# Optimization experiments

Hardware: AMD Instinct MI355X
Metric: run time of the kernel (lower is better)

The kernel has to match this reference:

```python
import jax, jax.numpy as jnp
import numpy as np

N = 100000      # nodes
E = 3200000     # edges
F_IN = 64       # num_input_features
HID = 3         # hardcoded hidden width in GCN
F_OUT = 256     # gcn_output_features
F_TR = 512      # transformer_feature_size


def setup_inputs() -> dict:
    key = jax.random.key(0)
    ks = jax.random.split(key, 12)
    x = jax.random.normal(ks[0], (N, F_IN), dtype=jnp.float32)
    edge_index = jax.random.randint(ks[1], (2, E), 0, N, dtype=jnp.int64)
    s = 0.05
    # ChebConv1 (K=2): two weight mats [in,out] + bias
    W0a = jax.random.normal(ks[2], (F_IN, HID), jnp.float32) * s
    W1a = jax.random.normal(ks[3], (F_IN, HID), jnp.float32) * s
    b1 = jax.random.normal(ks[4], (HID,), jnp.float32) * s
    # ChebConv2 (K=2)
    W0b = jax.random.normal(ks[5], (HID, F_OUT), jnp.float32) * s
    W1b = jax.random.normal(ks[6], (HID, F_OUT), jnp.float32) * s
    b2 = jax.random.normal(ks[7], (F_OUT,), jnp.float32) * s
    # final Linear
    Wl = jax.random.normal(ks[8], (F_OUT, F_TR), jnp.float32) * s
    bl = jax.random.normal(ks[9], (F_TR,), jnp.float32) * s
    return {"x": x, "edge_index": edge_index, "W0a": W0a, "W1a": W1a,
            "b1": b1, "W0b": W0b, "W1b": W1b, "b2": b2, "Wl": Wl, "bl": bl}


def _cheb_norm(edge_index, num_nodes):
    # PyG ChebConv.__norm__ with sym normalization, lambda_max=2.0:
    # L_hat = 2L/2 - I = -D^{-1/2} A D^{-1/2} (diagonal cancels to 0).
    src, dst = edge_index[0], edge_index[1]
    w = jnp.where(src != dst, 1.0, 0.0).astype(jnp.float32)  # remove_self_loops
    deg = jnp.zeros((num_nodes,), jnp.float32).at[src].add(w)
    dinv = jnp.where(deg > 0, jax.lax.rsqrt(jnp.maximum(deg, 1.0)), 0.0)
    return -dinv[src] * w * dinv[dst]  # [E]


def _cheb_conv(x, edge_index, norm, W0, W1, b):
    # K=2 Chebyshev: Tx0 = x, Tx1 = L_hat @ x (scatter-add over edges)
    src, dst = edge_index[0], edge_index[1]
    Tx1 = jnp.zeros_like(x).at[dst].add(norm[:, None] * x[src])
    return x @ W0 + Tx1 @ W1 + b


def reference(x, edge_index, W0a, W1a, b1, W0b, W1b, b2, Wl, bl):
    norm = _cheb_norm(edge_index, x.shape[0])
    h = jax.nn.relu(_cheb_conv(x, edge_index, norm, W0a, W1a, b1))
    h = jax.nn.relu(_cheb_conv(h, edge_index, norm, W0b, W1b, b2))
    return h @ Wl + bl
```

## Files before the change

kernel.cpp:

```cpp
#include <hip/hip_runtime.h>
#include <hip/hip_bf16.h>


#define MAXNB 1024
#define BSH 7
#define BSZ 128
#define SRC_BITS 20
#define SRC_MASK ((1u << SRC_BITS) - 1u)
#define EPB 16384

typedef __attribute__((ext_vector_type(8))) short short8;
typedef __attribute__((ext_vector_type(4))) float f32x4;

static __device__ inline unsigned short f2bf(float f) {
    union { float f; unsigned u; } v; v.f = f;
    unsigned r = (v.u + 0x7fffu + ((v.u >> 16) & 1u)) >> 16;
    return (unsigned short)r;
}

__global__ __launch_bounds__(256) void k_prep(const float* __restrict__ Wl,
                                              unsigned short* __restrict__ WlT,
                                              unsigned* __restrict__ subcurD,
                                              unsigned* __restrict__ subcurS) {
    __shared__ float tile[32][33];
    int t = threadIdx.x, tx = t & 31, ty = t >> 5;
    if (blockIdx.x == 0) {
        for (int i = t; i < MAXNB; i += 256) { subcurD[i] = 0u; subcurS[i] = 0u; }
    }
    int kb = (blockIdx.x & 7) * 32;
    int cb = (blockIdx.x >> 3) * 32;
#pragma unroll
    for (int r = 0; r < 4; r++) {
        int k = kb + ty + r * 8;
        tile[ty + r * 8][tx] = Wl[(size_t)k * 512 + cb + tx];
    }
    __syncthreads();
#pragma unroll
    for (int r = 0; r < 4; r++) {
        int c = cb + ty + r * 8;
        WlT[(size_t)c * 256 + kb + tx] = f2bf(tile[tx][ty + r * 8]);
    }
}

__global__ __launch_bounds__(1024) void k_hist(const int* __restrict__ ei, int E, int NB,
                                               unsigned* __restrict__ subcurD,
                                               unsigned* __restrict__ subcurS,
                                               unsigned* __restrict__ baseD,
                                               unsigned* __restrict__ baseS) {
    __shared__ unsigned hD[MAXNB], hS[MAXNB];
    int t = threadIdx.x, blk = blockIdx.x;
    for (int i = t; i < NB; i += 1024) { hD[i] = 0u; hS[i] = 0u; }
    __syncthreads();
    int e0 = blk * EPB, e1 = min(e0 + EPB, E);
    if ((E & 3) == 0) {
        int nv = (e1 - e0) >> 2;
        const int4* s4 = (const int4*)(ei + e0);
        const int4* d4 = (const int4*)(ei + (size_t)E + e0);
        for (int i = t; i < nv; i += 1024) {
            int4 ss = s4[i], dd = d4[i];
            if (ss.x != dd.x) { atomicAdd(&hD[dd.x >> BSH], 1u); atomicAdd(&hS[ss.x >> BSH], 1u); }
            if (ss.y != dd.y) { atomicAdd(&hD[dd.y >> BSH], 1u); atomicAdd(&hS[ss.y >> BSH], 1u); }
            if (ss.z != dd.z) { atomicAdd(&hD[dd.z >> BSH], 1u); atomicAdd(&hS[ss.z >> BSH], 1u); }
            if (ss.w != dd.w) { atomicAdd(&hD[dd.w >> BSH], 1u); atomicAdd(&hS[ss.w >> BSH], 1u); }
        }
        for (int e = e0 + (nv << 2) + t; e < e1; e += 1024) {
            int s = ei[e], d = ei[(size_t)E + e];
            if (s != d) { atomicAdd(&hD[d >> BSH], 1u); atomicAdd(&hS[s >> BSH], 1u); }
        }
    } else {
        for (int e = e0 + t; e < e1; e += 1024) {
            int s = ei[e], d = ei[(size_t)E + e];
            if (s != d) { atomicAdd(&hD[d >> BSH], 1u); atomicAdd(&hS[s >> BSH], 1u); }
        }
    }
    __syncthreads();
    unsigned* bD = baseD + (size_t)blk * NB;
    unsigned* bS = baseS + (size_t)blk * NB;
    for (int i = t; i < NB; i += 1024) {
        unsigned h = hD[i];
        if (h) bD[i] = atomicAdd(&subcurD[i], h);
        h = hS[i];
        if (h) bS[i] = atomicAdd(&subcurS[i], h);
    }
}

__global__ __launch_bounds__(1024) void k_scan(const unsigned* __restrict__ totD,
                                               const unsigned* __restrict__ totS,
                                               unsigned* __restrict__ startD,
                                               unsigned* __restrict__ startS, int NB) {
    __shared__ unsigned a[MAXNB], b[MAXNB];
    int t = threadIdx.x;
    for (int i = t; i < NB; i += 1024) a[i] = totD[i];
    __syncthreads();
    unsigned* s = a; unsigned* d = b;
    for (int off = 1; off < NB; off <<= 1) {
        for (int i = t; i < NB; i += 1024)
            d[i] = s[i] + (i >= off ? s[i - off] : 0u);
        __syncthreads();
        unsigned* tmp = s; s = d; d = tmp;
    }
    for (int i = t; i < NB; i += 1024)
        startD[i] = (i == 0) ? 0u : s[i - 1];
    if (t == 0) startD[NB] = s[NB - 1];
    __syncthreads();
    for (int i = t; i < NB; i += 1024) a[i] = totS[i];
    __syncthreads();
    s = a; d = b;
    for (int off = 1; off < NB; off <<= 1) {
        for (int i = t; i < NB; i += 1024)
            d[i] = s[i] + (i >= off ? s[i - off] : 0u);
        __syncthreads();
        unsigned* tmp = s; s = d; d = tmp;
    }
    for (int i = t; i < NB; i += 1024)
        startS[i] = (i == 0) ? 0u : s[i - 1];
    if (t == 0) startS[NB] = s[NB - 1];
}

__global__ __launch_bounds__(1024) void k_place(const int* __restrict__ ei, int E, int NB,
                                                const unsigned* __restrict__ startD,
                                                const unsigned* __restrict__ startS,
                                                const unsigned* __restrict__ baseD,
                                                const unsigned* __restrict__ baseS,
                                                unsigned* __restrict__ dstbin,
                                                unsigned char* __restrict__ srcbin) {
    __shared__ unsigned oD[MAXNB], oS[MAXNB], cD[MAXNB], cS[MAXNB];
    int t = threadIdx.x, blk = blockIdx.x;
    const unsigned* bD = baseD + (size_t)blk * NB;
    const unsigned* bS = baseS + (size_t)blk * NB;
    for (int i = t; i < NB; i += 1024) {
        oD[i] = startD[i] + bD[i];
        oS[i] = startS[i] + bS[i];
        cD[i] = 0u; cS[i] = 0u;
    }
    __syncthreads();
    int e0 = blk * EPB, e1 = min(e0 + EPB, E);
    if ((E & 3) == 0) {
        int nv = (e1 - e0) >> 2;
        const int4* s4 = (const int4*)(ei + e0);
        const int4* d4 = (const int4*)(ei + (size_t)E + e0);
        for (int i = t; i < nv; i += 1024) {
            int4 ss = s4[i], dd = d4[i];
            int sa[4] = {ss.x, ss.y, ss.z, ss.w};
            int da[4] = {dd.x, dd.y, dd.z, dd.w};
#pragma unroll
            for (int j = 0; j < 4; j++) {
                int s = sa[j], d = da[j];
                if (s != d) {
                    int bk = d >> BSH;
                    unsigned pos = oD[bk] + atomicAdd(&cD[bk], 1u);
                    dstbin[pos] = ((unsigned)(d & (BSZ - 1)) << SRC_BITS) | (unsigned)s;
                    int bs = s >> BSH;
                    unsigned ps = oS[bs] + atomicAdd(&cS[bs], 1u);
                    srcbin[ps] = (unsigned char)(s & (BSZ - 1));
                }
            }
        }
        for (int e = e0 + (nv << 2) + t; e < e1; e += 1024) {
            int s = ei[e], d = ei[(size_t)E + e];
            if (s != d) {
                int bk = d >> BSH;
                unsigned pos = oD[bk] + atomicAdd(&cD[bk], 1u);
                dstbin[pos] = ((unsigned)(d & (BSZ - 1)) << SRC_BITS) | (unsigned)s;
                int bs = s >> BSH;
                unsigned ps = oS[bs] + atomicAdd(&cS[bs], 1u);
                srcbin[ps] = (unsigned char)(s & (BSZ - 1));
            }
        }
    } else {
        for (int e = e0 + t; e < e1; e += 1024) {
            int s = ei[e], d = ei[(size_t)E + e];
            if (s != d) {
                int bk = d >> BSH;
                unsigned pos = oD[bk] + atomicAdd(&cD[bk], 1u);
                dstbin[pos] = ((unsigned)(d & (BSZ - 1)) << SRC_BITS) | (unsigned)s;
                int bs = s >> BSH;
                unsigned ps = oS[bs] + atomicAdd(&cS[bs], 1u);
                srcbin[ps] = (unsigned char)(s & (BSZ - 1));
            }
        }
    }
}

__global__ __launch_bounds__(256) void k_sortdeg(
    const unsigned* __restrict__ dstbin, const unsigned* __restrict__ startD,
    unsigned* __restrict__ dsorted, unsigned* __restrict__ nodeoff,
    const unsigned char* __restrict__ srcbin, const unsigned* __restrict__ startS,
    const float* __restrict__ x, const float* __restrict__ W0a,
    const float* __restrict__ W1a, float* __restrict__ dinv,
    float4* __restrict__ a3v, float4* __restrict__ y3v, int N) {
    __shared__ unsigned cnt[BSZ], tmp[BSZ], cur[BSZ];
    __shared__ unsigned cnt4[4][BSZ];
    __shared__ float w0[192], w1[192];
    __shared__ float dl[BSZ];
    int t = threadIdx.x, b = blockIdx.x;
    if (t < 192) { w0[t] = W0a[t]; w1[t] = W1a[t]; }
    if (t < BSZ) cnt[t] = 0u;
    for (int i = t; i < 4 * BSZ; i += 256) ((unsigned*)cnt4)[i] = 0u;
    __syncthreads();
    unsigned d0 = startD[b], d1 = startD[b + 1];
    for (unsigned e = d0 + t; e < d1; e += 256)
        atomicAdd(&cnt[dstbin[e] >> SRC_BITS], 1u);
    unsigned s0 = startS[b], s1 = startS[b + 1];
    int rep = t & 3;
    for (unsigned i = s0 + t; i < s1; i += 256) atomicAdd(&cnt4[rep][srcbin[i]], 1u);
    __syncthreads();
    for (int off = 1; off < BSZ; off <<= 1) {
        if (t < BSZ) tmp[t] = cnt[t] + (t >= off ? cnt[t - off] : 0u);
        __syncthreads();
        if (t < BSZ) cnt[t] = tmp[t];
        __syncthreads();
    }
    if (t <= BSZ) {
        unsigned ex = (t == 0) ? 0u : cnt[t - 1];
        int idx = b * BSZ + t;
        if (idx <= N) nodeoff[idx] = d0 + ex;
        if (t < BSZ) cur[t] = ex;
    }
    __syncthreads();
    for (unsigned e = d0 + t; e < d1; e += 256) {
        unsigned p = dstbin[e];
        unsigned pos = d0 + atomicAdd(&cur[p >> SRC_BITS], 1u);
        dsorted[pos] = p & SRC_MASK;
    }
    if (t < BSZ) {
        unsigned c = cnt4[0][t] + cnt4[1][t] + cnt4[2][t] + cnt4[3][t];
        float dv = c ? rsqrtf((float)c) : 0.f;
        dl[t] = dv;
        int g = b * BSZ + t;
        if (g < N) dinv[g] = dv;
    }
    __syncthreads();
    int q = t & 3;
#pragma unroll
    for (int pass = 0; pass < 2; pass++) {
        int nn = (t >> 2) + pass * 64;
        int node = b * BSZ + nn;
        float acc[6] = {0.f, 0.f, 0.f, 0.f, 0.f, 0.f};
        if (node < N) {
            const float4* xr = (const float4*)(x + (size_t)node * 64 + q * 16);
#pragma unroll
            for (int i = 0; i < 4; i++) {
                float4 v = xr[i];
                float xs[4] = {v.x, v.y, v.z, v.w};
#pragma unroll
                for (int c = 0; c < 4; c++) {
                    int f = q * 16 + i * 4 + c;
                    float xi = xs[c];
                    acc[0] += xi * w0[f * 3 + 0];
                    acc[1] += xi * w0[f * 3 + 1];
                    acc[2] += xi * w0[f * 3 + 2];
                    acc[3] += xi * w1[f * 3 + 0];
                    acc[4] += xi * w1[f * 3 + 1];
                    acc[5] += xi * w1[f * 3 + 2];
                }
            }
        }
#pragma unroll
        for (int m = 1; m < 4; m <<= 1)
#pragma unroll
            for (int j = 0; j < 6; j++) acc[j] += __shfl_xor(acc[j], m, 64);
        if (q == 0 && node < N) {
            a3v[node] = make_float4(acc[0], acc[1], acc[2], 0.f);
            y3v[node] = make_float4(acc[3], acc[4], acc[5], dl[nn]);
        }
    }
}

__global__ __launch_bounds__(512) void k_tgather(
    const unsigned* __restrict__ dsorted, const unsigned* __restrict__ nodeoff,
    const float4* __restrict__ v4, const float* __restrict__ dinv,
    const float4* __restrict__ a3v, const float* __restrict__ b1,
    float4* __restrict__ outv, int N) {
    int t = threadIdx.x;
    int g = t >> 3, q = t & 7;
    int node = blockIdx.x * 64 + g;
    if (node >= N) return;
    float dv = dinv[node];
    unsigned o0 = nodeoff[node], o1 = nodeoff[node + 1];
    float s0 = 0.f, s1 = 0.f, s2 = 0.f;
    for (unsigned e = o0 + q; e < o1; e += 8) {
        float4 v = v4[dsorted[e]];
        float nm = -v.w * dv;
        s0 += nm * v.x; s1 += nm * v.y; s2 += nm * v.z;
    }
#pragma unroll
    for (int m = 1; m < 8; m <<= 1) {
        s0 += __shfl_xor(s0, m, 64);
        s1 += __shfl_xor(s1, m, 64);
        s2 += __shfl_xor(s2, m, 64);
    }
    if (q == 0) {
        float4 a = a3v[node];
        outv[node] = make_float4(fmaxf(s0 + a.x + b1[0], 0.f),
                                 fmaxf(s1 + a.y + b1[1], 0.f),
                                 fmaxf(s2 + a.z + b1[2], 0.f), dv);
    }
}

__global__ __launch_bounds__(256) void k_final_mfma(
    const float4* __restrict__ h1v, const unsigned* __restrict__ dsorted,
    const unsigned* __restrict__ nodeoff,
    const float* __restrict__ W0b, const float* __restrict__ W1b,
    const float* __restrict__ b2, const unsigned short* __restrict__ WlT,
    const float* __restrict__ bl, float* __restrict__ out, int N) {
    __shared__ unsigned short h2s[64 * 256];
    __shared__ float4 u4[64][2];
    __shared__ float dl[64];
    char* h2b = (char*)h2s;
    int t = threadIdx.x, b = blockIdx.x;
    int n0 = b * 64;

    if (t < 64) {
        int g = n0 + t;
        float4 hv = (g < N) ? h1v[g] : make_float4(0.f, 0.f, 0.f, 0.f);
        u4[t][0] = hv;
        dl[t] = hv.w;
    }
    __syncthreads();

    {
        int g = t >> 2, q = t & 3;
        int node = n0 + g;
        float s0 = 0.f, s1 = 0.f, s2 = 0.f;
        if (node < N) {
            float dv = dl[g];
            unsigned o0 = nodeoff[node], o1 = nodeoff[node + 1];
            for (unsigned e = o0 + q; e < o1; e += 4) {
                float4 v = h1v[dsorted[e]];
                float nm = -v.w * dv;
                s0 += nm * v.x; s1 += nm * v.y; s2 += nm * v.z;
            }
        }
#pragma unroll
        for (int m = 1; m < 4; m <<= 1) {
            s0 += __shfl_xor(s0, m, 64);
            s1 += __shfl_xor(s1, m, 64);
            s2 += __shfl_xor(s2, m, 64);
        }
        if (q == 0) u4[g][1] = make_float4(s0, s1, s2, 0.f);
    }
    __syncthreads();

    {
        int k0 = (t & 127) * 2;
        int rh = (t >> 7) * 32;
        float w00a = W0b[k0],       w00b = W0b[k0 + 1];
        float w01a = W0b[256 + k0], w01b = W0b[256 + k0 + 1];
        float w02a = W0b[512 + k0], w02b = W0b[512 + k0 + 1];
        float w10a = W1b[k0],       w10b = W1b[k0 + 1];
        float w11a = W1b[256 + k0], w11b = W1b[256 + k0 + 1];
        float w12a = W1b[512 + k0], w12b = W1b[512 + k0 + 1];
        float bka = b2[k0], bkb = b2[k0 + 1];
        int kbyte = k0 * 2;
#pragma unroll
        for (int r = 0; r < 32; r++) {
            int rr = rh + r;
            float4 h = u4[rr][0];
            float4 v = u4[rr][1];
            float za = bka + h.x * w00a + h.y * w01a + h.z * w02a
                           + v.x * w10a + v.y * w11a + v.z * w12a;
            float zb = bkb + h.x * w00b + h.y * w01b + h.z * w02b
                           + v.x * w10b + v.y * w11b + v.z * w12b;
            za = fmaxf(za, 0.f); zb = fmaxf(zb, 0.f);
            unsigned pk = ((unsigned)f2bf(zb) << 16) | (unsigned)f2bf(za);
            int byte = rr * 512 + (kbyte ^ ((rr & 7) << 4));
            *(unsigned*)(h2b + byte) = pk;
        }
    }
    __syncthreads();

    int w = t >> 6, l = t & 63;
    int col0 = w * 128;
    int lrow = l & 15, lkb = (l >> 4) * 8, cq = (l >> 4) * 4;

#pragma unroll
    for (int ch = 0; ch < 2; ch++) {
        int cb0 = col0 + ch * 64;
        f32x4 acc[4][4];
#pragma unroll
        for (int rt = 0; rt < 4; rt++)
#pragma unroll
            for (int ct = 0; ct < 4; ct++) acc[rt][ct] = (f32x4)0.f;

#pragma unroll
        for (int ks = 0; ks < 8; ks++) {
            int kel = ks * 32 + lkb;
            short8 af[4];
#pragma unroll
            for (int rt = 0; rt < 4; rt++) {
                int r = rt * 16 + lrow;
                int byte = r * 512 + ((kel * 2) ^ ((r & 7) << 4));
                af[rt] = *(const short8*)(h2b + byte);
            }
            short8 bf[4];
#pragma unroll
            for (int ct = 0; ct < 4; ct++) {
                int c = cb0 + ct * 16 + lrow;
                bf[ct] = *(const short8*)(WlT + (size_t)c * 256 + kel);
            }
#pragma unroll
            for (int rt = 0; rt < 4; rt++)
#pragma unroll
                for (int ct = 0; ct < 4; ct++)
                    acc[rt][ct] = __builtin_amdgcn_mfma_f32_16x16x32_bf16(
                        bf[ct], af[rt], acc[rt][ct], 0, 0, 0);
        }

        f32x4 blv[4];
#pragma unroll
        for (int ct = 0; ct < 4; ct++)
            blv[ct] = *(const f32x4*)(bl + cb0 + ct * 16 + cq);
#pragma unroll
        for (int rt = 0; rt < 4; rt++) {
            int row = n0 + rt * 16 + lrow;
            if (row < N) {
                float* orow = out + (size_t)row * 512 + cb0 + cq;
#pragma unroll
                for (int ct = 0; ct < 4; ct++) {
                    f32x4 sv = acc[rt][ct] + blv[ct];
                    __builtin_nontemporal_store(sv, (f32x4*)(orow + ct * 16));
                }
            }
        }
    }
}

extern "C" void kernel_launch(void* const* d_in, const int* in_sizes, int n_in,
                              void* d_out, int out_size, void* d_ws, size_t ws_size,
                              hipStream_t stream) {
    const float* x   = (const float*)d_in[0];
    const int*   ei  = (const int*)d_in[1];
    const float* W0a = (const float*)d_in[2];
    const float* W1a = (const float*)d_in[3];
    const float* b1  = (const float*)d_in[4];
    const float* W0b = (const float*)d_in[5];
    const float* W1b = (const float*)d_in[6];
    const float* b2  = (const float*)d_in[7];
    const float* Wl  = (const float*)d_in[8];
    const float* bl  = (const float*)d_in[9];
    float* out = (float*)d_out;

    const int N = in_sizes[0] / 64;
    const int E = in_sizes[1] / 2;
    const int NB = (N + BSZ - 1) >> BSH;
    const int CB = (E + EPB - 1) / EPB;
    const int NB64 = (N + 63) / 64;

    char* base = (char*)d_ws;
    size_t off = 0;
    auto alloc = [&](size_t bytes) {
        void* p = base + off;
        off = (off + bytes + 255) & ~(size_t)255;
        return p;
    };
    unsigned* subcurD = (unsigned*)alloc(MAXNB * 4);
    unsigned* subcurS = (unsigned*)alloc(MAXNB * 4);
    unsigned* startD  = (unsigned*)alloc((MAXNB + 1) * 4);
    unsigned* startS  = (unsigned*)alloc((MAXNB + 1) * 4);
    unsigned* baseD   = (unsigned*)alloc((size_t)CB * NB * 4);
    unsigned* baseS   = (unsigned*)alloc((size_t)CB * NB * 4);
    unsigned* dstbin  = (unsigned*)alloc((size_t)E * 4);
    unsigned* dsorted = (unsigned*)alloc((size_t)E * 4);
    unsigned* nodeoff = (unsigned*)alloc((size_t)(N + 1) * 4);
    unsigned char* srcbin = (unsigned char*)alloc((size_t)E);
    float* dinv = (float*)alloc((size_t)N * 4);
    float* a3v  = (float*)alloc((size_t)N * 16);
    float* y3v  = (float*)alloc((size_t)N * 16);
    float* h1v  = (float*)alloc((size_t)N * 16);
    unsigned short* WlT = (unsigned short*)alloc(512 * 256 * 2);

    k_prep<<<128, 256, 0, stream>>>(Wl, WlT, subcurD, subcurS);
    k_hist<<<CB, 1024, 0, stream>>>(ei, E, NB, subcurD, subcurS, baseD, baseS);
    k_scan<<<1, 1024, 0, stream>>>(subcurD, subcurS, startD, startS, NB);
    k_place<<<CB, 1024, 0, stream>>>(ei, E, NB, startD, startS, baseD, baseS,
                                     dstbin, srcbin);
    k_sortdeg<<<NB, 256, 0, stream>>>(dstbin, startD, dsorted, nodeoff,
                                      srcbin, startS, x, W0a, W1a, dinv,
                                      (float4*)a3v, (float4*)y3v, N);
    k_tgather<<<NB64, 512, 0, stream>>>(dsorted, nodeoff, (const float4*)y3v, dinv,
                                        (const float4*)a3v, b1, (float4*)h1v, N);
    k_final_mfma<<<NB64, 256, 0, stream>>>(
        (const float4*)h1v, dsorted, nodeoff, W0b, W1b, b2, WlT, bl, out, N);
}
```

Measured before the change: 237.7 us.

## Split second-layer edge gather out of final MFMA kernel and shrink its tile

The second ChebConv neighbor aggregation is moved out of the final GEMM kernel into a second launch of the gather kernel, which writes a per-node float4 buffer. The final kernel now only loads the two precomputed float4s per node and handles 32 nodes per block instead of 64, halving LDS use and accumulator registers so more blocks can be resident. This is meant to stop the latency-bound irregular gather from stalling the MFMA/store-heavy kernel. The cost is an extra launch, an extra N*16-byte buffer round trip, and WlT reloaded twice as often per output row. Output stores also switch from nontemporal to ordinary stores.

```diff
diff --git a/kernel.cpp b/kernel.cpp
--- a/kernel.cpp
+++ b/kernel.cpp
@@ -271,7 +271,7 @@
     const unsigned* __restrict__ dsorted, const unsigned* __restrict__ nodeoff,
     const float4* __restrict__ v4, const float* __restrict__ dinv,
     const float4* __restrict__ a3v, const float* __restrict__ b1,
-    float4* __restrict__ outv, int N) {
+    float4* __restrict__ outv, int N, int phase) {
     int t = threadIdx.x;
     int g = t >> 3, q = t & 7;
     int node = blockIdx.x * 64 + g;
@@ -291,60 +291,40 @@
         s2 += __shfl_xor(s2, m, 64);
     }
     if (q == 0) {
-        float4 a = a3v[node];
-        outv[node] = make_float4(fmaxf(s0 + a.x + b1[0], 0.f),
-                                 fmaxf(s1 + a.y + b1[1], 0.f),
-                                 fmaxf(s2 + a.z + b1[2], 0.f), dv);
+        if (phase == 1) {
+            float4 a = a3v[node];
+            outv[node] = make_float4(fmaxf(s0 + a.x + b1[0], 0.f),
+                                     fmaxf(s1 + a.y + b1[1], 0.f),
+                                     fmaxf(s2 + a.z + b1[2], 0.f), dv);
+        } else {
+            outv[node] = make_float4(s0, s1, s2, 0.f);
+        }
     }
 }
 
 __global__ __launch_bounds__(256) void k_final_mfma(
-    const float4* __restrict__ h1v, const unsigned* __restrict__ dsorted,
-    const unsigned* __restrict__ nodeoff,
+    const float4* __restrict__ h1v, const float4* __restrict__ t2r,
     const float* __restrict__ W0b, const float* __restrict__ W1b,
     const float* __restrict__ b2, const unsigned short* __restrict__ WlT,
     const float* __restrict__ bl, float* __restrict__ out, int N) {
-    __shared__ unsigned short h2s[64 * 256];
-    __shared__ float4 u4[64][2];
-    __shared__ float dl[64];
+    __shared__ unsigned short h2s[32 * 256];
+    __shared__ float4 u4[32][2];
     char* h2b = (char*)h2s;
     int t = threadIdx.x, b = blockIdx.x;
-    int n0 = b * 64;
-
-    if (t < 64) {
+    int n0 = b * 32;
+
+    if (t < 32) {
         int g = n0 + t;
-        float4 hv = (g < N) ? h1v[g] : make_float4(0.f, 0.f, 0.f, 0.f);
-        u4[t][0] = hv;
-        dl[t] = hv.w;
-    }
-    __syncthreads();
-
-    {
-        int g = t >> 2, q = t & 3;
-        int node = n0 + g;
-        float s0 = 0.f, s1 = 0.f, s2 = 0.f;
-        if (node < N) {
-            float dv = dl[g];
-            unsigned o0 = nodeoff[node], o1 = nodeoff[node + 1];
-            for (unsigned e = o0 + q; e < o1; e += 4) {
-                float4 v = h1v[dsorted[e]];
-                float nm = -v.w * dv;
-                s0 += nm * v.x; s1 += nm * v.y; s2 += nm * v.z;
-            }
-        }
-#pragma unroll
-        for (int m = 1; m < 4; m <<= 1) {
-            s0 += __shfl_xor(s0, m, 64);
-            s1 += __shfl_xor(s1, m, 64);
-            s2 += __shfl_xor(s2, m, 64);
-        }
-        if (q == 0) u4[g][1] = make_float4(s0, s1, s2, 0.f);
+        u4[t][0] = (g < N) ? h1v[g] : make_float4(0.f, 0.f, 0.f, 0.f);
+    } else if (t < 64) {
+        int g = n0 + t - 32;
+        u4[t - 32][1] = (g < N) ? t2r[g] : make_float4(0.f, 0.f, 0.f, 0.f);
     }
     __syncthreads();
 
     {
         int k0 = (t & 127) * 2;
-        int rh = (t >> 7) * 32;
+        int rh = (t >> 7) * 16;
         float w00a = W0b[k0],       w00b = W0b[k0 + 1];
         float w01a = W0b[256 + k0], w01b = W0b[256 + k0 + 1];
         float w02a = W0b[512 + k0], w02b = W0b[512 + k0 + 1];
@@ -354,7 +334,7 @@
         float bka = b2[k0], bkb = b2[k0 + 1];
         int kbyte = k0 * 2;
 #pragma unroll
-        for (int r = 0; r < 32; r++) {
+        for (int r = 0; r < 16; r++) {
             int rr = rh + r;
             float4 h = u4[rr][0];
             float4 v = u4[rr][1];
@@ -377,18 +357,18 @@
 #pragma unroll
     for (int ch = 0; ch < 2; ch++) {
         int cb0 = col0 + ch * 64;
-        f32x4 acc[4][4];
-#pragma unroll
-        for (int rt = 0; rt < 4; rt++)
+        f32x4 acc[2][4];
+#pragma unroll
+        for (int rt = 0; rt < 2; rt++)
 #pragma unroll
             for (int ct = 0; ct < 4; ct++) acc[rt][ct] = (f32x4)0.f;
 
 #pragma unroll
         for (int ks = 0; ks < 8; ks++) {
             int kel = ks * 32 + lkb;
-            short8 af[4];
-#pragma unroll
-            for (int rt = 0; rt < 4; rt++) {
+            short8 af[2];
+#pragma unroll
+            for (int rt = 0; rt < 2; rt++) {
                 int r = rt * 16 + lrow;
                 int byte = r * 512 + ((kel * 2) ^ ((r & 7) << 4));
                 af[rt] = *(const short8*)(h2b + byte);
@@ -400,7 +380,7 @@
                 bf[ct] = *(const short8*)(WlT + (size_t)c * 256 + kel);
             }
 #pragma unroll
-            for (int rt = 0; rt < 4; rt++)
+            for (int rt = 0; rt < 2; rt++)
 #pragma unroll
                 for (int ct = 0; ct < 4; ct++)
                     acc[rt][ct] = __builtin_amdgcn_mfma_f32_16x16x32_bf16(
@@ -412,14 +392,14 @@
         for (int ct = 0; ct < 4; ct++)
             blv[ct] = *(const f32x4*)(bl + cb0 + ct * 16 + cq);
 #pragma unroll
-        for (int rt = 0; rt < 4; rt++) {
+        for (int rt = 0; rt < 2; rt++) {
             int row = n0 + rt * 16 + lrow;
             if (row < N) {
                 float* orow = out + (size_t)row * 512 + cb0 + cq;
 #pragma unroll
                 for (int ct = 0; ct < 4; ct++) {
                     f32x4 sv = acc[rt][ct] + blv[ct];
-                    __builtin_nontemporal_store(sv, (f32x4*)(orow + ct * 16));
+                    *(f32x4*)(orow + ct * 16) = sv;
                 }
             }
         }
@@ -446,6 +426,7 @@
     const int NB = (N + BSZ - 1) >> BSH;
     const int CB = (E + EPB - 1) / EPB;
     const int NB64 = (N + 63) / 64;
+    const int NB32 = (N + 31) / 32;
 
     char* base = (char*)d_ws;
     size_t off = 0;
@@ -468,6 +449,7 @@
     float* a3v  = (float*)alloc((size_t)N * 16);
     float* y3v  = (float*)alloc((size_t)N * 16);
     float* h1v  = (float*)alloc((size_t)N * 16);
+    float* t2r  = (float*)alloc((size_t)N * 16);
     unsigned short* WlT = (unsigned short*)alloc(512 * 256 * 2);
 
     k_prep<<<128, 256, 0, stream>>>(Wl, WlT, subcurD, subcurS);
@@ -479,7 +461,9 @@
                                       srcbin, startS, x, W0a, W1a, dinv,
                                       (float4*)a3v, (float4*)y3v, N);
     k_tgather<<<NB64, 512, 0, stream>>>(dsorted, nodeoff, (const float4*)y3v, dinv,
-                                        (const float4*)a3v, b1, (float4*)h1v, N);
-    k_final_mfma<<<NB64, 256, 0, stream>>>(
-        (const float4*)h1v, dsorted, nodeoff, W0b, W1b, b2, WlT, bl, out, N);
-}
+                                        (const float4*)a3v, b1, (float4*)h1v, N, 1);
+    k_tgather<<<NB64, 512, 0, stream>>>(dsorted, nodeoff, (const float4*)h1v, dinv,
+                                        (const float4*)a3v, b1, (float4*)t2r, N, 2);
+    k_final_mfma<<<NB32, 256, 0, stream>>>(
+        (const float4*)h1v, (const float4*)t2r, W0b, W1b, b2, WlT, bl, out, N);
+}
```

New measurement: 254.3 us. 1.07x slower.
